# Kernel optimization log

Measured on AMD Instinct MI355X. Metric: run time of the kernel, lower is better.

## Reference

```python
import jax, jax.numpy as jnp
import numpy as np

S, HID = 2048, 4096
H, KV, D = 32, 8, 128
EPS = 1e-6
THETA = 10000.0


def setup_inputs() -> dict:
    key = jax.random.key(0)
    k0, k1, k2 = jax.random.split(key, 3)
    return {
        "positions": jnp.arange(S, dtype=jnp.int32),
        "hidden_states": jax.random.normal(k0, (S, HID), jnp.float32),
        "w_qkv": jax.random.normal(k1, ((H + 2 * KV) * D, HID), jnp.float32) * 0.02,
        "w_o": jax.random.normal(k2, (HID, H * D), jnp.float32) * 0.02,
        "gq": jnp.ones((D,), jnp.float32),
        "gk": jnp.ones((D,), jnp.float32),
    }


def _rmsnorm(x, g):
    # per-head RMSNorm over last dim (head_dim)
    return x * jax.lax.rsqrt(jnp.mean(x * x, axis=-1, keepdims=True) + EPS) * g


def _rope(x, positions):
    # NeoX-style rotary embedding, rotary_dim == head_dim
    half = D // 2
    inv_freq = 1.0 / (THETA ** (jnp.arange(half, dtype=jnp.float32) * 2.0 / D))
    freqs = positions.astype(jnp.float32)[:, None] * inv_freq  # [S, half]
    cos = jnp.cos(freqs)[:, None, :]  # [S, 1, half]
    sin = jnp.sin(freqs)[:, None, :]
    x1, x2 = x[..., :half], x[..., half:]
    return jnp.concatenate([x1 * cos - x2 * sin, x2 * cos + x1 * sin], axis=-1)


def reference(positions, hidden_states, w_qkv, w_o, gq, gk):
    qkv = hidden_states @ w_qkv.T  # [S, (H+2KV)*D]
    q = qkv[:, : H * D].reshape(S, H, D)
    k = qkv[:, H * D : (H + KV) * D].reshape(S, KV, D)
    v = qkv[:, (H + KV) * D :].reshape(S, KV, D)

    q = _rmsnorm(q, gq)
    k = _rmsnorm(k, gk)
    q = _rope(q, positions)
    k = _rope(k, positions)

    rep = H // KV
    kf = jnp.repeat(k, rep, axis=1)  # [S, H, D]
    vf = jnp.repeat(v, rep, axis=1)

    scale = D ** -0.5
    scores = jnp.einsum("qhd,khd->hqk", q, kf) * scale  # [H, S, S]
    causal = jnp.tril(jnp.ones((S, S), dtype=bool))
    scores = jnp.where(causal[None], scores, jnp.finfo(scores.dtype).min)
    attn = jax.nn.softmax(scores, axis=-1)
    ctx = jnp.einsum("hqk,khd->qhd", attn, vf).reshape(S, H * D)
    return ctx @ w_o.T  # [S, HID]
```

## Files before the change

kernel.cpp:

```cpp
#include <hip/hip_runtime.h>
#include <hip/hip_bf16.h>

#define S_LEN 2048
#define HID   4096
#define NH    32
#define NKV   8
#define DH    128
#define NQKV  ((NH + 2*NKV) * DH)

typedef __attribute__((ext_vector_type(8))) short s16x8;
typedef __attribute__((ext_vector_type(4))) short s16x4;
typedef __attribute__((ext_vector_type(4))) float f32x4;

__device__ __forceinline__ short f2bf(float x) {
    union { __hip_bfloat16 b; short s; } u;
    u.b = __float2bfloat16(x);
    return u.s;
}
__device__ __forceinline__ float bf2f(short s) {
    union { unsigned int u; float f; } v;
    v.u = ((unsigned int)(unsigned short)s) << 16;
    return v.f;
}

__device__ __forceinline__ void gload16(const void* g, void* l) {
    __builtin_amdgcn_global_load_lds(
        (const __attribute__((address_space(1))) void*)g,
        (__attribute__((address_space(3))) void*)l,
        16, 0, 0);
}

__device__ __forceinline__ void cstore(float* p, float v) { *p = v; }
__device__ __forceinline__ void cstore(short* p, float v) { *p = f2bf(v); }

__global__ __launch_bounds__(256) void convert_hs_wqkv(
        const float* __restrict__ in1, short* __restrict__ o1, long n1,
        const float* __restrict__ in2, short* __restrict__ o2, long n2)
{
    const long total = n1 + n2;
    long i0 = ((long)blockIdx.x * blockDim.x + threadIdx.x) * 4;
    long stride = (long)gridDim.x * blockDim.x * 4;
    for (long i = i0; i < total; i += stride) {
        const float* src; short* dst; long off;
        if (i < n1) { src = in1; dst = o1; off = i; }
        else        { src = in2; dst = o2; off = i - n1; }
        float4 v = *(const float4*)(src + off);
        s16x4 o;
        o[0] = f2bf(v.x); o[1] = f2bf(v.y); o[2] = f2bf(v.z); o[3] = f2bf(v.w);
        *(s16x4*)(dst + off) = o;
    }
}

template <typename OT>
__global__ __launch_bounds__(256, 2) void gemm192(
        const short* __restrict__ A, const short* __restrict__ B,
        OT* __restrict__ C, int M, int N, int K)
{
    __shared__ char lds[81920];
    const int t = threadIdx.x;
    const int w = t >> 6, l = t & 63, g = l >> 4, q16 = l & 15;
    const int wm = w >> 1, wn = w & 1;
    const int bx = blockIdx.x, by = blockIdx.y;
    const int NT = K >> 6;

    const int srow = t >> 3;
    const int schunk = (t & 7) ^ (srow & 7);
    unsigned goffA[4], goffB[6];
#pragma unroll
    for (int i = 0; i < 4; ++i)
        goffA[i] = (unsigned)(((by * 128 + i * 32 + srow) * K) * 2 + schunk * 16);
#pragma unroll
    for (int i = 0; i < 6; ++i)
        goffB[i] = (unsigned)(((bx * 192 + i * 32 + srow) * K) * 2 + schunk * 16);
    const int dstw = w * 1024;

    auto STAGE = [&](int kt) {
        const int par = kt & 1;
        char* dA = lds + par * 16384 + dstw;
        char* dB = lds + 32768 + par * 24576 + dstw;
        const unsigned kb = (unsigned)kt * 128;
#pragma unroll
        for (int i = 0; i < 4; ++i)
            gload16((const char*)A + (goffA[i] + kb), dA + i * 4096);
#pragma unroll
        for (int i = 0; i < 6; ++i)
            gload16((const char*)B + (goffB[i] + kb), dB + i * 4096);
    };

    int aoff[4], boff[6];
#pragma unroll
    for (int mi = 0; mi < 4; ++mi) aoff[mi] = (wm * 64 + mi * 16 + q16) * 128;
#pragma unroll
    for (int ni = 0; ni < 6; ++ni) boff[ni] = (wn * 96 + ni * 16 + q16) * 128;
    const int sw0 = ((g) ^ (q16 & 7)) << 4;
    const int sw1 = ((4 + g) ^ (q16 & 7)) << 4;

    f32x4 acc[4][6] = {};
    s16x8 aE[4][2], aO[4][2], b0f[3][2], b1f[3][2];

    STAGE(0); STAGE(1);
    asm volatile("s_waitcnt vmcnt(10)" ::: "memory");
    __builtin_amdgcn_s_barrier();
    {
        const char* A0 = lds;
#pragma unroll
        for (int mi = 0; mi < 4; ++mi) {
            aE[mi][0] = *(const s16x8*)(A0 + aoff[mi] + sw0);
            aE[mi][1] = *(const s16x8*)(A0 + aoff[mi] + sw1);
        }
    }

#define GB(KT, AC, AN, PAR) do {                                              \
    const char* Bs_ = lds + 32768 + (PAR) * 24576;                            \
    _Pragma("unroll")                                                         \
    for (int ni = 0; ni < 3; ++ni) {                                          \
        b0f[ni][0] = *(const s16x8*)(Bs_ + boff[ni] + sw0);                   \
        b0f[ni][1] = *(const s16x8*)(Bs_ + boff[ni] + sw1);                   \
    }                                                                         \
    _Pragma("unroll")                                                         \
    for (int ni = 0; ni < 3; ++ni) {                                          \
        b1f[ni][0] = *(const s16x8*)(Bs_ + boff[3 + ni] + sw0);               \
        b1f[ni][1] = *(const s16x8*)(Bs_ + boff[3 + ni] + sw1);               \
    }                                                                         \
    asm volatile("s_waitcnt lgkmcnt(6)" ::: "memory");       \
    __builtin_amdgcn_sched_barrier(0);                                        \
    __builtin_amdgcn_s_setprio(1);                                            \
    _Pragma("unroll")                                                         \
    for (int mi = 0; mi < 4; ++mi)                                            \
    _Pragma("unroll")                                                         \
    for (int ni = 0; ni < 3; ++ni)                                            \
    _Pragma("unroll")                                                         \
    for (int kk = 0; kk < 2; ++kk)                                            \
        acc[mi][ni] = __builtin_amdgcn_mfma_f32_16x16x32_bf16(                \
                AC[mi][kk], b0f[ni][kk], acc[mi][ni], 0, 0, 0);               \
    __builtin_amdgcn_s_setprio(0);                                            \
    asm volatile("s_waitcnt lgkmcnt(0)" ::: "memory");           \
    __builtin_amdgcn_sched_barrier(0);                                        \
    asm volatile("s_waitcnt vmcnt(0)" ::: "memory");        \
    __builtin_amdgcn_s_barrier();       \
    if ((KT) + 2 < NT) STAGE((KT) + 2);                                       \
    if ((KT) + 1 < NT) {                      \
        const char* An_ = lds + (((PAR) ^ 1) * 16384);                        \
        _Pragma("unroll")                                                     \
        for (int mi = 0; mi < 4; ++mi) {                                      \
            AN[mi][0] = *(const s16x8*)(An_ + aoff[mi] + sw0);                \
            AN[mi][1] = *(const s16x8*)(An_ + aoff[mi] + sw1);                \
        }                                                                     \
    }                                                                         \
    __builtin_amdgcn_s_setprio(1);                                            \
    _Pragma("unroll")                                                         \
    for (int mi = 0; mi < 4; ++mi)                                            \
    _Pragma("unroll")                                                         \
    for (int ni = 0; ni < 3; ++ni)                                            \
    _Pragma("unroll")                                                         \
    for (int kk = 0; kk < 2; ++kk)                                            \
        acc[mi][3 + ni] = __builtin_amdgcn_mfma_f32_16x16x32_bf16(            \
                AC[mi][kk], b1f[ni][kk], acc[mi][3 + ni], 0, 0, 0);           \
    __builtin_amdgcn_s_setprio(0);                                            \
} while (0)

    for (int kt = 0; kt < NT; kt += 2) {
        GB(kt,     aE, aO, 0);
        GB(kt + 1, aO, aE, 1);
    }
#undef GB

#pragma unroll
    for (int mi = 0; mi < 4; ++mi) {
        long row = (long)by * 128 + wm * 64 + mi * 16 + g * 4;
#pragma unroll
        for (int ni = 0; ni < 6; ++ni) {
            long col = (long)bx * 192 + wn * 96 + ni * 16 + q16;
            f32x4 v = acc[mi][ni];
#pragma unroll
            for (int r = 0; r < 4; ++r)
                cstore(&C[(row + r) * (long)N + col], v[r]);
        }
    }
}

template <typename OT>
__global__ __launch_bounds__(512, 4) void gemm_bt(
        const short* __restrict__ A, const short* __restrict__ B,
        OT* __restrict__ C, int M, int N, int K)
{
    __shared__ char lds[64 * 1024];
    const int t = threadIdx.x;
    const int w = t >> 6, l = t & 63, g = l >> 4, q16 = l & 15;
    const int wm = w >> 2, wn = w & 3;
    const long rowA = (long)blockIdx.y * 128;
    const long rowB = (long)blockIdx.x * 128;
    const int NT = K >> 6;

    long goffA[2], goffB[2];
#pragma unroll
    for (int i = 0; i < 2; ++i) {
        int li = i * 512 + t;
        int row = li >> 3;
        int chunk = (t & 7) ^ (row & 7);
        goffA[i] = ((rowA + row) * (long)K) * 2 + chunk * 16;
        goffB[i] = ((rowB + row) * (long)K) * 2 + chunk * 16;
    }
    const int ldsoff = w * 1024;

    int aoff[4][2], boff[2][2];
#pragma unroll
    for (int m = 0; m < 4; ++m)
#pragma unroll
        for (int k = 0; k < 2; ++k) {
            int row = wm * 64 + m * 16 + q16;
            int chunk = (k * 4 + g) ^ (row & 7);
            aoff[m][k] = row * 128 + chunk * 16;
        }
#pragma unroll
    for (int n = 0; n < 2; ++n)
#pragma unroll
        for (int k = 0; k < 2; ++k) {
            int row = wn * 32 + n * 16 + q16;
            int chunk = (k * 4 + g) ^ (row & 7);
            boff[n][k] = row * 128 + chunk * 16;
        }

    auto STAGE = [&](int kt, char* dA, char* dB) {
        const long kb = (long)kt * 128;
#pragma unroll
        for (int i = 0; i < 2; ++i)
            gload16((const char*)A + goffA[i] + kb, dA + i * 8192 + ldsoff);
#pragma unroll
        for (int i = 0; i < 2; ++i)
            gload16((const char*)B + goffB[i] + kb, dB + i * 8192 + ldsoff);
    };

    f32x4 acc[4][2] = {};

    STAGE(0, lds, lds + 32768);
    STAGE(1, lds + 16384, lds + 49152);

    for (int kt = 0; kt < NT; ++kt) {
        const int b = kt & 1;
        char* bA = lds + (b ? 16384 : 0);
        char* bB = lds + (b ? 49152 : 32768);
        if (kt + 1 < NT) asm volatile("s_waitcnt vmcnt(4)" ::: "memory");
        else             asm volatile("s_waitcnt vmcnt(0)" ::: "memory");
        __builtin_amdgcn_s_barrier();

        s16x8 af[4][2], bfr[2][2];
#pragma unroll
        for (int m = 0; m < 4; ++m)
#pragma unroll
            for (int k = 0; k < 2; ++k)
                af[m][k] = *(const s16x8*)(bA + aoff[m][k]);
#pragma unroll
        for (int n = 0; n < 2; ++n)
#pragma unroll
            for (int k = 0; k < 2; ++k)
                bfr[n][k] = *(const s16x8*)(bB + boff[n][k]);

        __builtin_amdgcn_s_setprio(1);
#pragma unroll
        for (int m = 0; m < 4; ++m)
#pragma unroll
            for (int n = 0; n < 2; ++n)
#pragma unroll
                for (int k = 0; k < 2; ++k)
                    acc[m][n] = __builtin_amdgcn_mfma_f32_16x16x32_bf16(
                            af[m][k], bfr[n][k], acc[m][n], 0, 0, 0);
        __builtin_amdgcn_s_setprio(0);
        __builtin_amdgcn_s_barrier();

        if (kt + 2 < NT) STAGE(kt + 2, bA, bB);
    }

#pragma unroll
    for (int m = 0; m < 4; ++m) {
        long row = rowA + wm * 64 + m * 16 + g * 4;
#pragma unroll
        for (int n = 0; n < 2; ++n) {
            long col = rowB + wn * 32 + n * 16 + q16;
            f32x4 v = acc[m][n];
#pragma unroll
            for (int r = 0; r < 4; ++r)
                cstore(&C[(row + r) * (long)N + col], v[r]);
        }
    }
}

__global__ __launch_bounds__(256) void post_gemm1_fused(
        const float* __restrict__ wo, short* __restrict__ wob,
        const short* __restrict__ qkvb, const int* __restrict__ pos,
        const float* __restrict__ gq, const float* __restrict__ gk,
        short* __restrict__ qo, short* __restrict__ ko,
        short* __restrict__ vt)
{
    const int bid = blockIdx.x;

    if (bid < 2048) {
        const long n = (long)HID * (NH * DH);
        long i0 = ((long)bid * 256 + threadIdx.x) * 4;
        long stride = 2048L * 256 * 4;
        for (long i = i0; i < n; i += stride) {
            float4 v = *(const float4*)(wo + i);
            s16x4 o;
            o[0] = f2bf(v.x); o[1] = f2bf(v.y); o[2] = f2bf(v.z); o[3] = f2bf(v.w);
            *(s16x4*)(wob + i) = o;
        }
        return;
    }

    if (bid < 12288) {
        const int idx = bid - 2048;
        const int s = idx / 5;
        const int slot = (idx % 5) * 8 + (threadIdx.x >> 5);
        const int p = threadIdx.x & 31, d = p * 4;

        s16x4 xv = *(const s16x4*)(qkvb + (long)s * NQKV + slot * DH + d);
        float x[4];
#pragma unroll
        for (int r = 0; r < 4; ++r) x[r] = bf2f(xv[r]);

        float ss = x[0]*x[0] + x[1]*x[1] + x[2]*x[2] + x[3]*x[3];
#pragma unroll
        for (int o = 1; o < 32; o <<= 1) ss += __shfl_xor(ss, o);
        float rms = rsqrtf(ss * (1.0f / DH) + 1e-6f);

        const bool isq = slot < NH;
        const float* gp = isq ? gq : gk;
        float y[4];
#pragma unroll
        for (int r = 0; r < 4; ++r) y[r] = x[r] * rms * gp[d + r];

        float y2[4];
#pragma unroll
        for (int r = 0; r < 4; ++r) y2[r] = __shfl_xor(y[r], 16);

        const float po = (float)pos[s];
        const int jbase = d & 63;
        s16x4 ov;
#pragma unroll
        for (int r = 0; r < 4; ++r) {
            float invf = exp2f(-(float)(jbase + r) * (13.287712379549449f / 64.0f));
            float ang = po * invf;
            float c = cosf(ang), sn = sinf(ang);
            float outv = (d < 64) ? (y[r] * c - y2[r] * sn)
                                  : (y[r] * c + y2[r] * sn);
            ov[r] = f2bf(outv);
        }
        if (isq) *(s16x4*)(qo + ((long)s * NH + slot) * DH + d) = ov;
        else     *(s16x4*)(ko + ((long)s * NKV + (slot - NH)) * DH + d) = ov;
        return;
    }

    __shared__ short tile[64][72];
    const int idx2 = bid - 12288;
    const int sb = idx2 & 31, db = (idx2 >> 5) & 1, h = idx2 >> 6;
    const int t = threadIdx.x;
#pragma unroll
    for (int i = 0; i < 2; ++i) {
        int c = i * 256 + t;
        int row = c >> 3, dc = (c & 7) * 8;
        const short* src = qkvb + (long)(sb*64 + row) * NQKV
                           + (NH + NKV + h) * DH + db*64 + dc;
        s16x8 x = *(const s16x8*)src;
#pragma unroll
        for (int jj = 0; jj < 8; ++jj) tile[row][dc + jj] = x[jj];
    }
    __syncthreads();
#pragma unroll
    for (int i = 0; i < 2; ++i) {
        int c = i * 256 + t;
        int dr = c >> 3, sc = (c & 7) * 8;
        s16x8 y;
#pragma unroll
        for (int jj = 0; jj < 8; ++jj) y[jj] = tile[sc + jj][dr];
        short* dst = vt + (long)(h*DH + db*64 + dr) * S_LEN + sb*64 + sc;
        *(s16x8*)dst = y;
    }
}

__device__ __forceinline__ void stage_kv(const char* kgB, const char* vgB,
                                         int kt, int t, char* kd, char* vd)
{
    const int w = t >> 6;
#pragma unroll
    for (int ci = 0; ci < 4; ++ci) {
        int c = ci * 256 + t;
        int row = c >> 4, col16 = c & 15;
        const char* gk = kgB + (long)(kt*64 + row) * (NKV*DH*2)
                         + ((col16*16) ^ ((row & 7) << 4));
        gload16(gk, kd + ci*4096 + w*1024);
        int rowv = c >> 3, scol8 = c & 7;
        const char* gv = vgB + (long)rowv * (S_LEN*2) + kt*128
                         + ((scol8*16) ^ ((rowv & 7) << 4));
        gload16(gv, vd + ci*4096 + w*1024);
    }
}

__global__ __launch_bounds__(256, 2) void attn_kernel(
        const short* __restrict__ qg, const short* __restrict__ kg,
        const short* __restrict__ vtg, short* __restrict__ ctx)
{
    const int bx = blockIdx.x;
    const int h  = bx & 31;
    const int slot = bx >> 5;
    const int qb = (slot < 8) ? slot : 23 - slot;
    const int kvh = h >> 2;
    const int t = threadIdx.x, w = t >> 6, l = t & 63, g = l >> 4, q16 = l & 15;

    __shared__ char Kl[2][16384];
    __shared__ char Vl[2][16384];
    __shared__ short Pl[4][32 * 64];

    const float scale = 0.08838834764831845f;
    const char* kgB = (const char*)kg + (long)kvh * DH * 2;
    const char* vgB = (const char*)vtg + (long)kvh * DH * (long)S_LEN * 2;

    const int nt = 2 * qb + 2;
    int qrow[2];
    qrow[0] = qb*128 + w*32 + q16;
    qrow[1] = qrow[0] + 16;

    s16x8 qf[2][4];
#pragma unroll
    for (int s = 0; s < 2; ++s) {
        const short* qptr = qg + ((long)qrow[s] * NH + h) * DH;
#pragma unroll
        for (int dk = 0; dk < 4; ++dk)
            qf[s][dk] = *(const s16x8*)(qptr + dk*32 + g*8);
    }

    f32x4 oacc[2][8] = {};
    float m_run[2] = {-1e30f, -1e30f}, l_run[2] = {0.f, 0.f};

    stage_kv(kgB, vgB, 0, t, Kl[0], Vl[0]);
    __syncthreads();

    for (int kt = 0; kt < nt; ++kt) {
        const int b = kt & 1;
        if (kt + 1 < nt)
            stage_kv(kgB, vgB, kt + 1, t, Kl[b ^ 1], Vl[b ^ 1]);
        const char* kb = Kl[b];
        const char* vbb = Vl[b];

        f32x4 sacc[2][4] = {};
        __builtin_amdgcn_s_setprio(1);
#pragma unroll
        for (int m = 0; m < 4; ++m) {
            int kvr = m*16 + q16;
            s16x8 af[4];
#pragma unroll
            for (int dk = 0; dk < 4; ++dk) {
                int byte = (kvr*256 + (dk*32 + g*8)*2) ^ ((kvr & 7) << 4);
                af[dk] = *(const s16x8*)(kb + byte);
            }
#pragma unroll
            for (int s = 0; s < 2; ++s)
#pragma unroll
                for (int dk = 0; dk < 4; ++dk)
                    sacc[s][m] = __builtin_amdgcn_mfma_f32_16x16x32_bf16(
                            af[dk], qf[s][dk], sacc[s][m], 0,0,0);
        }
        __builtin_amdgcn_s_setprio(0);

        const bool diag = (kt >= 2*qb);
        float mx[2];
#pragma unroll
        for (int s = 0; s < 2; ++s) {
            mx[s] = -1e30f;
#pragma unroll
            for (int m = 0; m < 4; ++m)
#pragma unroll
                for (int r = 0; r < 4; ++r) {
                    float x = sacc[s][m][r] * scale;
                    if (diag) {
                        int kv = kt*64 + m*16 + g*4 + r;
                        if (kv > qrow[s]) x = -1e30f;
                    }
                    sacc[s][m][r] = x;
                    mx[s] = fmaxf(mx[s], x);
                }
            mx[s] = fmaxf(mx[s], __shfl_xor(mx[s], 16));
            mx[s] = fmaxf(mx[s], __shfl_xor(mx[s], 32));
        }
        if (__any((mx[0] > m_run[0] + 8.f) || (mx[1] > m_run[1] + 8.f))) {
#pragma unroll
            for (int s = 0; s < 2; ++s) {
                float m_new = fmaxf(m_run[s], mx[s]);
                float corr = __expf(m_run[s] - m_new);
                l_run[s] *= corr;
                m_run[s] = m_new;
                float rf[4];
#pragma unroll
                for (int r = 0; r < 4; ++r)
                    rf[r] = __shfl(corr, (g << 4) | (g*4 + r));
#pragma unroll
                for (int nf = 0; nf < 8; ++nf)
#pragma unroll
                    for (int r = 0; r < 4; ++r) oacc[s][nf][r] *= rf[r];
            }
        }
#pragma unroll
        for (int s = 0; s < 2; ++s) {
            float psum = 0.f;
#pragma unroll
            for (int m = 0; m < 4; ++m) {
                s16x4 pk;
#pragma unroll
                for (int r = 0; r < 4; ++r) {
                    float e = __expf(sacc[s][m][r] - m_run[s]);
                    psum += e;
                    pk[r] = f2bf(e);
                }
                int byte = ((s*16 + q16)*128 + (m*16 + g*4)*2) ^ ((q16 & 7) << 4);
                *(s16x4*)((char*)&Pl[w][0] + byte) = pk;
            }
            psum += __shfl_xor(psum, 16);
            psum += __shfl_xor(psum, 32);
            l_run[s] += psum;
        }

        __builtin_amdgcn_s_setprio(1);
#pragma unroll
        for (int ks = 0; ks < 2; ++ks) {
            s16x8 pa[2];
#pragma unroll
            for (int s = 0; s < 2; ++s) {
                int pbyte = ((s*16 + q16)*128 + (ks*32 + g*8)*2) ^ ((q16 & 7) << 4);
                pa[s] = *(const s16x8*)((const char*)&Pl[w][0] + pbyte);
            }
#pragma unroll
            for (int nf = 0; nf < 8; ++nf) {
                int drow = nf*16 + q16;
                int vbyte = (drow*128 + (ks*32 + g*8)*2) ^ ((drow & 7) << 4);
                s16x8 vbf = *(const s16x8*)(vbb + vbyte);
#pragma unroll
                for (int s = 0; s < 2; ++s)
                    oacc[s][nf] = __builtin_amdgcn_mfma_f32_16x16x32_bf16(
                            pa[s], vbf, oacc[s][nf], 0,0,0);
            }
        }
        __builtin_amdgcn_s_setprio(0);
        __syncthreads();
    }

#pragma unroll
    for (int s = 0; s < 2; ++s) {
        float lr[4];
#pragma unroll
        for (int r = 0; r < 4; ++r)
            lr[r] = __shfl(l_run[s], (g << 4) | (g*4 + r));
#pragma unroll
        for (int nf = 0; nf < 8; ++nf)
#pragma unroll
            for (int r = 0; r < 4; ++r) {
                int row = qb*128 + w*32 + s*16 + g*4 + r;
                int col = h*DH + nf*16 + q16;
                float val = oacc[s][nf][r] / lr[r];
                ctx[(long)row * (NH*DH) + col] = f2bf(val);
            }
    }
}

extern "C" void kernel_launch(void* const* d_in, const int* in_sizes, int n_in,
                              void* d_out, int out_size, void* d_ws, size_t ws_size,
                              hipStream_t stream)
{
    const int*   positions = (const int*)  d_in[0];
    const float* hs        = (const float*)d_in[1];
    const float* wqkv      = (const float*)d_in[2];
    const float* wo        = (const float*)d_in[3];
    const float* gq        = (const float*)d_in[4];
    const float* gk        = (const float*)d_in[5];
    float* out = (float*)d_out;
    char* ws = (char*)d_ws;

    const size_t MB = 1ull << 20;
    short* hsb   = (short*)(ws);
    short* ctxb  = (short*)(ws);
    short* wqkvb = (short*)(ws + 16*MB);
    short* wob   = (short*)(ws + 16*MB);
    short* vtbuf = (short*)(ws + 48*MB);
    short* qkvb  = (short*)(ws + 67*MB);
    short* qbuf  = (short*)(ws + 91*MB);
    short* kbuf  = (short*)(ws + 107*MB);

    (void)in_sizes; (void)n_in; (void)out_size; (void)ws_size;

    convert_hs_wqkv<<<2048, 256, 0, stream>>>(
            hs, hsb, (long)S_LEN * HID,
            wqkv, wqkvb, (long)NQKV * HID);
    gemm192<short><<<dim3(NQKV/192, S_LEN/128), 256, 0, stream>>>(
            hsb, wqkvb, qkvb, S_LEN, NQKV, HID);
    post_gemm1_fused<<<12800, 256, 0, stream>>>(
            wo, wob, qkvb, positions, gq, gk, qbuf, kbuf, vtbuf);
    attn_kernel<<<dim3(512), 256, 0, stream>>>(qbuf, kbuf, vtbuf, ctxb);
    gemm_bt<float><<<dim3(HID/128, S_LEN/128), 512, 0, stream>>>(
            ctxb, wob, out, S_LEN, HID, HID);
}
```

Before: 303.5 us.

## Fuse fp32-to-bf16 weight conversion into GEMM B-operand loads

Both GEMMs now read the fp32 weight matrices straight from global memory into registers, convert them to bf16, and write them into LDS. This replaces the separate conversion passes for w_qkv and w_o and their bf16 workspace copies. The A operand keeps the async global-to-LDS path. The cost is twice the global bytes for B per tile, register-staged loads instead of direct-to-LDS, and extra synchronisation in the main loop. The weights are also re-read by every row-block of tiles, so a tile's B fetch is no longer one bf16 read.

```diff
diff --git a/kernel.cpp b/kernel.cpp
--- a/kernel.cpp
+++ b/kernel.cpp
@@ -33,27 +33,22 @@
 __device__ __forceinline__ void cstore(float* p, float v) { *p = v; }
 __device__ __forceinline__ void cstore(short* p, float v) { *p = f2bf(v); }
 
-__global__ __launch_bounds__(256) void convert_hs_wqkv(
-        const float* __restrict__ in1, short* __restrict__ o1, long n1,
-        const float* __restrict__ in2, short* __restrict__ o2, long n2)
+__global__ __launch_bounds__(256) void convert_f32_bf16(
+        const float* __restrict__ in, short* __restrict__ o, long n)
 {
-    const long total = n1 + n2;
-    long i0 = ((long)blockIdx.x * blockDim.x + threadIdx.x) * 4;
-    long stride = (long)gridDim.x * blockDim.x * 4;
-    for (long i = i0; i < total; i += stride) {
-        const float* src; short* dst; long off;
-        if (i < n1) { src = in1; dst = o1; off = i; }
-        else        { src = in2; dst = o2; off = i - n1; }
-        float4 v = *(const float4*)(src + off);
-        s16x4 o;
-        o[0] = f2bf(v.x); o[1] = f2bf(v.y); o[2] = f2bf(v.z); o[3] = f2bf(v.w);
-        *(s16x4*)(dst + off) = o;
+    long i0 = ((long)blockIdx.x * 256 + threadIdx.x) * 4;
+    long stride = (long)gridDim.x * 256 * 4;
+    for (long i = i0; i < n; i += stride) {
+        float4 v = *(const float4*)(in + i);
+        s16x4 x;
+        x[0] = f2bf(v.x); x[1] = f2bf(v.y); x[2] = f2bf(v.z); x[3] = f2bf(v.w);
+        *(s16x4*)(o + i) = x;
     }
 }
 
 template <typename OT>
 __global__ __launch_bounds__(256, 2) void gemm192(
-        const short* __restrict__ A, const short* __restrict__ B,
+        const short* __restrict__ A, const float* __restrict__ Bf,
         OT* __restrict__ C, int M, int N, int K)
 {
     __shared__ char lds[81920];
@@ -65,26 +60,47 @@
 
     const int srow = t >> 3;
     const int schunk = (t & 7) ^ (srow & 7);
-    unsigned goffA[4], goffB[6];
+    unsigned goffA[4];
 #pragma unroll
     for (int i = 0; i < 4; ++i)
         goffA[i] = (unsigned)(((by * 128 + i * 32 + srow) * K) * 2 + schunk * 16);
-#pragma unroll
-    for (int i = 0; i < 6; ++i)
-        goffB[i] = (unsigned)(((bx * 192 + i * 32 + srow) * K) * 2 + schunk * 16);
+    unsigned gBf[6]; int wBoff[6];
+#pragma unroll
+    for (int i = 0; i < 6; ++i) {
+        int row = bx * 192 + i * 32 + srow;
+        gBf[i]  = (unsigned)(row * K) * 4 + (unsigned)schunk * 32;
+        wBoff[i] = (i * 32 + srow) * 128 + (t & 7) * 16;
+    }
     const int dstw = w * 1024;
 
-    auto STAGE = [&](int kt) {
-        const int par = kt & 1;
+    auto SA = [&](int kt, int par) {
         char* dA = lds + par * 16384 + dstw;
-        char* dB = lds + 32768 + par * 24576 + dstw;
         const unsigned kb = (unsigned)kt * 128;
 #pragma unroll
         for (int i = 0; i < 4; ++i)
             gload16((const char*)A + (goffA[i] + kb), dA + i * 4096);
-#pragma unroll
-        for (int i = 0; i < 6; ++i)
-            gload16((const char*)B + (goffB[i] + kb), dB + i * 4096);
+    };
+    float4 br[6][2];
+    auto LB = [&](int kt) {
+        const unsigned kb = (unsigned)kt * 256;
+#pragma unroll
+        for (int i = 0; i < 6; ++i) {
+            const char* p = (const char*)Bf + (gBf[i] + kb);
+            br[i][0] = *(const float4*)p;
+            br[i][1] = *(const float4*)(p + 16);
+        }
+    };
+    auto WB = [&](int par) {
+        char* dB = lds + 32768 + par * 24576;
+#pragma unroll
+        for (int i = 0; i < 6; ++i) {
+            s16x8 o;
+            o[0] = f2bf(br[i][0].x); o[1] = f2bf(br[i][0].y);
+            o[2] = f2bf(br[i][0].z); o[3] = f2bf(br[i][0].w);
+            o[4] = f2bf(br[i][1].x); o[5] = f2bf(br[i][1].y);
+            o[6] = f2bf(br[i][1].z); o[7] = f2bf(br[i][1].w);
+            *(s16x8*)(dB + wBoff[i]) = o;
+        }
     };
 
     int aoff[4], boff[6];
@@ -96,22 +112,24 @@
     const int sw1 = ((4 + g) ^ (q16 & 7)) << 4;
 
     f32x4 acc[4][6] = {};
-    s16x8 aE[4][2], aO[4][2], b0f[3][2], b1f[3][2];
-
-    STAGE(0); STAGE(1);
-    asm volatile("s_waitcnt vmcnt(10)" ::: "memory");
+    s16x8 af[4][2], b0f[3][2], b1f[3][2];
+
+    LB(0); SA(0, 0);
+    asm volatile("s_waitcnt vmcnt(4)" ::: "memory");
+    WB(0);
+    LB(1); SA(1, 1);
+    asm volatile("s_waitcnt vmcnt(16)" ::: "memory");
+    asm volatile("s_waitcnt lgkmcnt(0)" ::: "memory");
     __builtin_amdgcn_s_barrier();
-    {
-        const char* A0 = lds;
-#pragma unroll
-        for (int mi = 0; mi < 4; ++mi) {
-            aE[mi][0] = *(const s16x8*)(A0 + aoff[mi] + sw0);
-            aE[mi][1] = *(const s16x8*)(A0 + aoff[mi] + sw1);
-        }
-    }
-
-#define GB(KT, AC, AN, PAR) do {                                              \
+
+#define GB(KT, PAR) do {                                                      \
+    const char* As_ = lds + (PAR) * 16384;                                    \
     const char* Bs_ = lds + 32768 + (PAR) * 24576;                            \
+    _Pragma("unroll")                                                         \
+    for (int mi = 0; mi < 4; ++mi) {                                          \
+        af[mi][0] = *(const s16x8*)(As_ + aoff[mi] + sw0);                    \
+        af[mi][1] = *(const s16x8*)(As_ + aoff[mi] + sw1);                    \
+    }                                                                         \
     _Pragma("unroll")                                                         \
     for (int ni = 0; ni < 3; ++ni) {                                          \
         b0f[ni][0] = *(const s16x8*)(Bs_ + boff[ni] + sw0);                   \
@@ -122,7 +140,7 @@
         b1f[ni][0] = *(const s16x8*)(Bs_ + boff[3 + ni] + sw0);               \
         b1f[ni][1] = *(const s16x8*)(Bs_ + boff[3 + ni] + sw1);               \
     }                                                                         \
-    asm volatile("s_waitcnt lgkmcnt(6)" ::: "memory");       \
+    asm volatile("s_waitcnt lgkmcnt(6)" ::: "memory");      \
     __builtin_amdgcn_sched_barrier(0);                                        \
     __builtin_amdgcn_s_setprio(1);                                            \
     _Pragma("unroll")                                                         \
@@ -132,21 +150,16 @@
     _Pragma("unroll")                                                         \
     for (int kk = 0; kk < 2; ++kk)                                            \
         acc[mi][ni] = __builtin_amdgcn_mfma_f32_16x16x32_bf16(                \
-                AC[mi][kk], b0f[ni][kk], acc[mi][ni], 0, 0, 0);               \
+                af[mi][kk], b0f[ni][kk], acc[mi][ni], 0, 0, 0);               \
     __builtin_amdgcn_s_setprio(0);                                            \
     asm volatile("s_waitcnt lgkmcnt(0)" ::: "memory");           \
     __builtin_amdgcn_sched_barrier(0);                                        \
-    asm volatile("s_waitcnt vmcnt(0)" ::: "memory");        \
+    asm volatile("s_waitcnt vmcnt(0)" ::: "memory");     \
+    if ((KT) + 1 < NT) WB((PAR) ^ 1);                   \
+    asm volatile("s_waitcnt lgkmcnt(0)" ::: "memory");    \
+    __builtin_amdgcn_sched_barrier(0);                                        \
     __builtin_amdgcn_s_barrier();       \
-    if ((KT) + 2 < NT) STAGE((KT) + 2);                                       \
-    if ((KT) + 1 < NT) {                      \
-        const char* An_ = lds + (((PAR) ^ 1) * 16384);                        \
-        _Pragma("unroll")                                                     \
-        for (int mi = 0; mi < 4; ++mi) {                                      \
-            AN[mi][0] = *(const s16x8*)(An_ + aoff[mi] + sw0);                \
-            AN[mi][1] = *(const s16x8*)(An_ + aoff[mi] + sw1);                \
-        }                                                                     \
-    }                                                                         \
+    if ((KT) + 2 < NT) { LB((KT) + 2); SA((KT) + 2, (PAR)); }                 \
     __builtin_amdgcn_s_setprio(1);                                            \
     _Pragma("unroll")                                                         \
     for (int mi = 0; mi < 4; ++mi)                                            \
@@ -155,13 +168,13 @@
     _Pragma("unroll")                                                         \
     for (int kk = 0; kk < 2; ++kk)                                            \
         acc[mi][3 + ni] = __builtin_amdgcn_mfma_f32_16x16x32_bf16(            \
-                AC[mi][kk], b1f[ni][kk], acc[mi][3 + ni], 0, 0, 0);           \
+                af[mi][kk], b1f[ni][kk], acc[mi][3 + ni], 0, 0, 0);           \
     __builtin_amdgcn_s_setprio(0);                                            \
 } while (0)
 
     for (int kt = 0; kt < NT; kt += 2) {
-        GB(kt,     aE, aO, 0);
-        GB(kt + 1, aO, aE, 1);
+        GB(kt,     0);
+        GB(kt + 1, 1);
     }
 #undef GB
 
@@ -181,7 +194,7 @@
 
 template <typename OT>
 __global__ __launch_bounds__(512, 4) void gemm_bt(
-        const short* __restrict__ A, const short* __restrict__ B,
+        const short* __restrict__ A, const float* __restrict__ Bf,
         OT* __restrict__ C, int M, int N, int K)
 {
     __shared__ char lds[64 * 1024];
@@ -192,14 +205,16 @@
     const long rowB = (long)blockIdx.x * 128;
     const int NT = K >> 6;
 
-    long goffA[2], goffB[2];
+    long goffA[2];
+    unsigned gBf[2]; int wBoff[2];
 #pragma unroll
     for (int i = 0; i < 2; ++i) {
         int li = i * 512 + t;
         int row = li >> 3;
         int chunk = (t & 7) ^ (row & 7);
         goffA[i] = ((rowA + row) * (long)K) * 2 + chunk * 16;
-        goffB[i] = ((rowB + row) * (long)K) * 2 + chunk * 16;
+        gBf[i]   = (unsigned)((rowB + row) * (long)K) * 4 + (unsigned)chunk * 32;
+        wBoff[i] = row * 128 + (t & 7) * 16;
     }
     const int ldsoff = w * 1024;
 
@@ -221,26 +236,48 @@
             boff[n][k] = row * 128 + chunk * 16;
         }
 
-    auto STAGE = [&](int kt, char* dA, char* dB) {
+    auto SA = [&](int kt, char* dA) {
         const long kb = (long)kt * 128;
 #pragma unroll
         for (int i = 0; i < 2; ++i)
             gload16((const char*)A + goffA[i] + kb, dA + i * 8192 + ldsoff);
-#pragma unroll
-        for (int i = 0; i < 2; ++i)
-            gload16((const char*)B + goffB[i] + kb, dB + i * 8192 + ldsoff);
     };
+    float4 br[2][2];
+    auto LB = [&](int kt) {
+        const unsigned kb = (unsigned)kt * 256;
+#pragma unroll
+        for (int i = 0; i < 2; ++i) {
+            const char* p = (const char*)Bf + (gBf[i] + kb);
+            br[i][0] = *(const float4*)p;
+            br[i][1] = *(const float4*)(p + 16);
+        }
+    };
+    auto WB = [&](char* dB) {
+#pragma unroll
+        for (int i = 0; i < 2; ++i) {
+            s16x8 o;
+            o[0] = f2bf(br[i][0].x); o[1] = f2bf(br[i][0].y);
+            o[2] = f2bf(br[i][0].z); o[3] = f2bf(br[i][0].w);
+            o[4] = f2bf(br[i][1].x); o[5] = f2bf(br[i][1].y);
+            o[6] = f2bf(br[i][1].z); o[7] = f2bf(br[i][1].w);
+            *(s16x8*)(dB + wBoff[i]) = o;
+        }
+    };
 
     f32x4 acc[4][2] = {};
 
-    STAGE(0, lds, lds + 32768);
-    STAGE(1, lds + 16384, lds + 49152);
+    LB(0); SA(0, lds);
+    asm volatile("s_waitcnt vmcnt(2)" ::: "memory");
+    WB(lds + 32768);
+    LB(1); SA(1, lds + 16384);
+    asm volatile("s_waitcnt lgkmcnt(0)" ::: "memory");
 
     for (int kt = 0; kt < NT; ++kt) {
         const int b = kt & 1;
-        char* bA = lds + (b ? 16384 : 0);
-        char* bB = lds + (b ? 49152 : 32768);
-        if (kt + 1 < NT) asm volatile("s_waitcnt vmcnt(4)" ::: "memory");
+        char* bA  = lds + (b ? 16384 : 0);
+        char* bB  = lds + (b ? 49152 : 32768);
+        char* bB2 = lds + (b ? 32768 : 49152);
+        if (kt + 1 < NT) asm volatile("s_waitcnt vmcnt(6)" ::: "memory");
         else             asm volatile("s_waitcnt vmcnt(0)" ::: "memory");
         __builtin_amdgcn_s_barrier();
 
@@ -266,9 +303,15 @@
                     acc[m][n] = __builtin_amdgcn_mfma_f32_16x16x32_bf16(
                             af[m][k], bfr[n][k], acc[m][n], 0, 0, 0);
         __builtin_amdgcn_s_setprio(0);
+
+        if (kt + 1 < NT) {
+            asm volatile("s_waitcnt vmcnt(2)" ::: "memory");
+            WB(bB2);
+            asm volatile("s_waitcnt lgkmcnt(0)" ::: "memory");
+        }
         __builtin_amdgcn_s_barrier();
 
-        if (kt + 2 < NT) STAGE(kt + 2, bA, bB);
+        if (kt + 2 < NT) { LB(kt + 2); SA(kt + 2, bA); }
     }
 
 #pragma unroll
@@ -286,7 +329,6 @@
 }
 
 __global__ __launch_bounds__(256) void post_gemm1_fused(
-        const float* __restrict__ wo, short* __restrict__ wob,
         const short* __restrict__ qkvb, const int* __restrict__ pos,
         const float* __restrict__ gq, const float* __restrict__ gk,
         short* __restrict__ qo, short* __restrict__ ko,
@@ -294,21 +336,8 @@
 {
     const int bid = blockIdx.x;
 
-    if (bid < 2048) {
-        const long n = (long)HID * (NH * DH);
-        long i0 = ((long)bid * 256 + threadIdx.x) * 4;
-        long stride = 2048L * 256 * 4;
-        for (long i = i0; i < n; i += stride) {
-            float4 v = *(const float4*)(wo + i);
-            s16x4 o;
-            o[0] = f2bf(v.x); o[1] = f2bf(v.y); o[2] = f2bf(v.z); o[3] = f2bf(v.w);
-            *(s16x4*)(wob + i) = o;
-        }
-        return;
-    }
-
-    if (bid < 12288) {
-        const int idx = bid - 2048;
+    if (bid < 10240) {
+        const int idx = bid;
         const int s = idx / 5;
         const int slot = (idx % 5) * 8 + (threadIdx.x >> 5);
         const int p = threadIdx.x & 31, d = p * 4;
@@ -351,7 +380,7 @@
     }
 
     __shared__ short tile[64][72];
-    const int idx2 = bid - 12288;
+    const int idx2 = bid - 10240;
     const int sb = idx2 & 31, db = (idx2 >> 5) & 1, h = idx2 >> 6;
     const int t = threadIdx.x;
 #pragma unroll
@@ -576,23 +605,19 @@
     const size_t MB = 1ull << 20;
     short* hsb   = (short*)(ws);
     short* ctxb  = (short*)(ws);
-    short* wqkvb = (short*)(ws + 16*MB);
-    short* wob   = (short*)(ws + 16*MB);
-    short* vtbuf = (short*)(ws + 48*MB);
-    short* qkvb  = (short*)(ws + 67*MB);
-    short* qbuf  = (short*)(ws + 91*MB);
-    short* kbuf  = (short*)(ws + 107*MB);
+    short* qkvb  = (short*)(ws + 16*MB);
+    short* qbuf  = (short*)(ws + 40*MB);
+    short* kbuf  = (short*)(ws + 56*MB);
+    short* vtbuf = (short*)(ws + 60*MB);
 
     (void)in_sizes; (void)n_in; (void)out_size; (void)ws_size;
 
-    convert_hs_wqkv<<<2048, 256, 0, stream>>>(
-            hs, hsb, (long)S_LEN * HID,
-            wqkv, wqkvb, (long)NQKV * HID);
+    convert_f32_bf16<<<1024, 256, 0, stream>>>(hs, hsb, (long)S_LEN * HID);
     gemm192<short><<<dim3(NQKV/192, S_LEN/128), 256, 0, stream>>>(
-            hsb, wqkvb, qkvb, S_LEN, NQKV, HID);
-    post_gemm1_fused<<<12800, 256, 0, stream>>>(
-            wo, wob, qkvb, positions, gq, gk, qbuf, kbuf, vtbuf);
+            hsb, wqkv, qkvb, S_LEN, NQKV, HID);
+    post_gemm1_fused<<<10752, 256, 0, stream>>>(
+            qkvb, positions, gq, gk, qbuf, kbuf, vtbuf);
     attn_kernel<<<dim3(512), 256, 0, stream>>>(qbuf, kbuf, vtbuf, ctxb);
     gemm_bt<float><<<dim3(HID/128, S_LEN/128), 512, 0, stream>>>(
-            ctxb, wob, out, S_LEN, HID, HID);
-}
+            ctxb, wo, out, S_LEN, HID, HID);
+}
```

New measurement: 341.9 us. +12.7%, slower.

## Rewrite output-projection GEMM with 4-wave 64x64 warp tiles and A-fragment prefetch

Applied to the files above, without the earlier changes.

The final ctx @ w_o^T GEMM moves from 512 threads (8 waves, 64x32 warp tiles) to 256 threads (4 waves, 64x64 warp tiles), so each wave reuses more of its fragments per MFMA. The loop is rebuilt with ping-pong A register fragments that are prefetched from the next LDS stage while the second half of the MFMAs run, plus explicit lgkmcnt waits and sched barriers, mirroring the gemm192 structure. This aims to cut LDS traffic per MFMA and hide LDS latency. In exchange it uses more registers per thread and leaves fewer waves to hide latency. Global offsets are now 32-bit unsigned.

```diff
diff --git a/kernel.cpp b/kernel.cpp
--- a/kernel.cpp
+++ b/kernel.cpp
@@ -180,104 +180,120 @@
 }
 
 template <typename OT>
-__global__ __launch_bounds__(512, 4) void gemm_bt(
+__global__ __launch_bounds__(256, 2) void gemm_bt(
         const short* __restrict__ A, const short* __restrict__ B,
         OT* __restrict__ C, int M, int N, int K)
 {
-    __shared__ char lds[64 * 1024];
+    __shared__ char lds[65536];
     const int t = threadIdx.x;
     const int w = t >> 6, l = t & 63, g = l >> 4, q16 = l & 15;
-    const int wm = w >> 2, wn = w & 3;
-    const long rowA = (long)blockIdx.y * 128;
-    const long rowB = (long)blockIdx.x * 128;
+    const int wm = w >> 1, wn = w & 1;
+    const int bx = blockIdx.x, by = blockIdx.y;
     const int NT = K >> 6;
 
-    long goffA[2], goffB[2];
-#pragma unroll
-    for (int i = 0; i < 2; ++i) {
-        int li = i * 512 + t;
-        int row = li >> 3;
-        int chunk = (t & 7) ^ (row & 7);
-        goffA[i] = ((rowA + row) * (long)K) * 2 + chunk * 16;
-        goffB[i] = ((rowB + row) * (long)K) * 2 + chunk * 16;
-    }
-    const int ldsoff = w * 1024;
-
-    int aoff[4][2], boff[2][2];
-#pragma unroll
-    for (int m = 0; m < 4; ++m)
-#pragma unroll
-        for (int k = 0; k < 2; ++k) {
-            int row = wm * 64 + m * 16 + q16;
-            int chunk = (k * 4 + g) ^ (row & 7);
-            aoff[m][k] = row * 128 + chunk * 16;
-        }
-#pragma unroll
-    for (int n = 0; n < 2; ++n)
-#pragma unroll
-        for (int k = 0; k < 2; ++k) {
-            int row = wn * 32 + n * 16 + q16;
-            int chunk = (k * 4 + g) ^ (row & 7);
-            boff[n][k] = row * 128 + chunk * 16;
-        }
-
-    auto STAGE = [&](int kt, char* dA, char* dB) {
-        const long kb = (long)kt * 128;
-#pragma unroll
-        for (int i = 0; i < 2; ++i)
-            gload16((const char*)A + goffA[i] + kb, dA + i * 8192 + ldsoff);
-#pragma unroll
-        for (int i = 0; i < 2; ++i)
-            gload16((const char*)B + goffB[i] + kb, dB + i * 8192 + ldsoff);
+    const int srow = t >> 3;
+    const int schunk = (t & 7) ^ (srow & 7);
+    unsigned goffA[4], goffB[4];
+#pragma unroll
+    for (int i = 0; i < 4; ++i) {
+        goffA[i] = (unsigned)(((by * 128 + i * 32 + srow) * K) * 2 + schunk * 16);
+        goffB[i] = (unsigned)(((bx * 128 + i * 32 + srow) * K) * 2 + schunk * 16);
+    }
+    const int dstw = w * 1024;
+
+    auto STAGE = [&](int kt) {
+        const int par = kt & 1;
+        char* dA = lds + par * 16384 + dstw;
+        char* dB = lds + 32768 + par * 16384 + dstw;
+        const unsigned kb = (unsigned)kt * 128;
+#pragma unroll
+        for (int i = 0; i < 4; ++i) {
+            gload16((const char*)A + (goffA[i] + kb), dA + i * 4096);
+            gload16((const char*)B + (goffB[i] + kb), dB + i * 4096);
+        }
     };
 
-    f32x4 acc[4][2] = {};
-
-    STAGE(0, lds, lds + 32768);
-    STAGE(1, lds + 16384, lds + 49152);
-
-    for (int kt = 0; kt < NT; ++kt) {
-        const int b = kt & 1;
-        char* bA = lds + (b ? 16384 : 0);
-        char* bB = lds + (b ? 49152 : 32768);
-        if (kt + 1 < NT) asm volatile("s_waitcnt vmcnt(4)" ::: "memory");
-        else             asm volatile("s_waitcnt vmcnt(0)" ::: "memory");
-        __builtin_amdgcn_s_barrier();
-
-        s16x8 af[4][2], bfr[2][2];
-#pragma unroll
-        for (int m = 0; m < 4; ++m)
-#pragma unroll
-            for (int k = 0; k < 2; ++k)
-                af[m][k] = *(const s16x8*)(bA + aoff[m][k]);
-#pragma unroll
-        for (int n = 0; n < 2; ++n)
-#pragma unroll
-            for (int k = 0; k < 2; ++k)
-                bfr[n][k] = *(const s16x8*)(bB + boff[n][k]);
-
-        __builtin_amdgcn_s_setprio(1);
-#pragma unroll
-        for (int m = 0; m < 4; ++m)
-#pragma unroll
-            for (int n = 0; n < 2; ++n)
-#pragma unroll
-                for (int k = 0; k < 2; ++k)
-                    acc[m][n] = __builtin_amdgcn_mfma_f32_16x16x32_bf16(
-                            af[m][k], bfr[n][k], acc[m][n], 0, 0, 0);
-        __builtin_amdgcn_s_setprio(0);
-        __builtin_amdgcn_s_barrier();
-
-        if (kt + 2 < NT) STAGE(kt + 2, bA, bB);
-    }
-
-#pragma unroll
-    for (int m = 0; m < 4; ++m) {
-        long row = rowA + wm * 64 + m * 16 + g * 4;
-#pragma unroll
-        for (int n = 0; n < 2; ++n) {
-            long col = rowB + wn * 32 + n * 16 + q16;
-            f32x4 v = acc[m][n];
+    int aoff[4], boff[4];
+#pragma unroll
+    for (int i = 0; i < 4; ++i) {
+        aoff[i] = (wm * 64 + i * 16 + q16) * 128;
+        boff[i] = (wn * 64 + i * 16 + q16) * 128;
+    }
+    const int sw0 = ((g) ^ (q16 & 7)) << 4;
+    const int sw1 = ((4 + g) ^ (q16 & 7)) << 4;
+
+    f32x4 acc[4][4] = {};
+    s16x8 aE[4][2], aO[4][2], bf[4][2];
+
+    STAGE(0); STAGE(1);
+    asm volatile("s_waitcnt vmcnt(8)" ::: "memory");
+    __builtin_amdgcn_s_barrier();
+    {
+        const char* A0 = lds;
+#pragma unroll
+        for (int mi = 0; mi < 4; ++mi) {
+            aE[mi][0] = *(const s16x8*)(A0 + aoff[mi] + sw0);
+            aE[mi][1] = *(const s16x8*)(A0 + aoff[mi] + sw1);
+        }
+    }
+
+#define GB(KT, AC, AN, PAR) do {                                              \
+    const char* Bs_ = lds + 32768 + (PAR) * 16384;                            \
+    _Pragma("unroll")                                                         \
+    for (int ni = 0; ni < 4; ++ni) {                                          \
+        bf[ni][0] = *(const s16x8*)(Bs_ + boff[ni] + sw0);                    \
+        bf[ni][1] = *(const s16x8*)(Bs_ + boff[ni] + sw1);                    \
+    }                                                                         \
+    asm volatile("s_waitcnt lgkmcnt(4)" ::: "memory");      \
+    __builtin_amdgcn_sched_barrier(0);                                        \
+    __builtin_amdgcn_s_setprio(1);                                            \
+    _Pragma("unroll")                                                         \
+    for (int mi = 0; mi < 4; ++mi)                                            \
+    _Pragma("unroll")                                                         \
+    for (int ni = 0; ni < 2; ++ni)                                            \
+    _Pragma("unroll")                                                         \
+    for (int kk = 0; kk < 2; ++kk)                                            \
+        acc[mi][ni] = __builtin_amdgcn_mfma_f32_16x16x32_bf16(                \
+                AC[mi][kk], bf[ni][kk], acc[mi][ni], 0, 0, 0);                \
+    __builtin_amdgcn_s_setprio(0);                                            \
+    asm volatile("s_waitcnt lgkmcnt(0)" ::: "memory");          \
+    __builtin_amdgcn_sched_barrier(0);                                        \
+    asm volatile("s_waitcnt vmcnt(0)" ::: "memory");        \
+    __builtin_amdgcn_s_barrier();       \
+    if ((KT) + 2 < NT) STAGE((KT) + 2);                                       \
+    if ((KT) + 1 < NT) {                      \
+        const char* An_ = lds + (((PAR) ^ 1) * 16384);                        \
+        _Pragma("unroll")                                                     \
+        for (int mi = 0; mi < 4; ++mi) {                                      \
+            AN[mi][0] = *(const s16x8*)(An_ + aoff[mi] + sw0);                \
+            AN[mi][1] = *(const s16x8*)(An_ + aoff[mi] + sw1);                \
+        }                                                                     \
+    }                                                                         \
+    __builtin_amdgcn_s_setprio(1);                                            \
+    _Pragma("unroll")                                                         \
+    for (int mi = 0; mi < 4; ++mi)                                            \
+    _Pragma("unroll")                                                         \
+    for (int ni = 0; ni < 2; ++ni)                                            \
+    _Pragma("unroll")                                                         \
+    for (int kk = 0; kk < 2; ++kk)                                            \
+        acc[mi][2 + ni] = __builtin_amdgcn_mfma_f32_16x16x32_bf16(            \
+                AC[mi][kk], bf[2 + ni][kk], acc[mi][2 + ni], 0, 0, 0);        \
+    __builtin_amdgcn_s_setprio(0);                                            \
+} while (0)
+
+    for (int kt = 0; kt < NT; kt += 2) {
+        GB(kt,     aE, aO, 0);
+        GB(kt + 1, aO, aE, 1);
+    }
+#undef GB
+
+#pragma unroll
+    for (int mi = 0; mi < 4; ++mi) {
+        long row = (long)by * 128 + wm * 64 + mi * 16 + g * 4;
+#pragma unroll
+        for (int ni = 0; ni < 4; ++ni) {
+            long col = (long)bx * 128 + wn * 64 + ni * 16 + q16;
+            f32x4 v = acc[mi][ni];
 #pragma unroll
             for (int r = 0; r < 4; ++r)
                 cstore(&C[(row + r) * (long)N + col], v[r]);
@@ -593,6 +609,6 @@
     post_gemm1_fused<<<12800, 256, 0, stream>>>(
             wo, wob, qkvb, positions, gq, gk, qbuf, kbuf, vtbuf);
     attn_kernel<<<dim3(512), 256, 0, stream>>>(qbuf, kbuf, vtbuf, ctxb);
-    gemm_bt<float><<<dim3(HID/128, S_LEN/128), 512, 0, stream>>>(
+    gemm_bt<float><<<dim3(HID/128, S_LEN/128), 256, 0, stream>>>(
             ctxb, wob, out, S_LEN, HID, HID);
 }
```

After: 299.9 us. No clear change (-1.2%).
